# Optimization experiments

Measured on AMD Instinct MI355X. Metric: run time of the kernel, lower is better.

## Reference

```python
import jax, jax.numpy as jnp
import numpy as np

B, S, H = 32, 4096, 1024


def setup_inputs() -> dict:
    key = jax.random.key(0)
    k1, k2, k3, k4 = jax.random.split(key, 4)
    hidden = jax.random.normal(k1, (B, 1, H), dtype=jnp.float32)
    encoder_outputs = jax.random.normal(k2, (B, S, H), dtype=jnp.float32)
    # nn.Linear(H, H): weight [H, H], bias [H]; scaled like torch default-ish init
    W = jax.random.normal(k3, (H, H), dtype=jnp.float32) / np.sqrt(H)
    b = jax.random.normal(k4, (H,), dtype=jnp.float32) / np.sqrt(H)
    return {"hidden": hidden, "encoder_outputs": encoder_outputs, "W": W, "b": b}


def reference(hidden, encoder_outputs, W, b):
    # method == 'general': energy_i = Linear(enc_i); score_i = hidden[:,0] . energy_i
    energy = jnp.einsum('bsh,kh->bsk', encoder_outputs, W) + b  # [B,S,H]
    attn_energies = jnp.einsum('bh,bsh->bs', hidden[:, 0], energy)  # [B,S]
    return jax.nn.softmax(attn_energies, axis=1)
```

## Files before the change

kernel.cpp:

```cpp
#include <hip/hip_runtime.h>
#include <math.h>

#define BB 32
#define SS 4096
#define HH 1024

__global__ __launch_bounds__(256) void compute_v_kernel(
        const float* __restrict__ hidden,
        const float* __restrict__ W,
        float* __restrict__ v) {
    const int b = blockIdx.y;
    const int h = blockIdx.x * 256 + threadIdx.x;
    const float* __restrict__ hb = hidden + b * HH;
    float acc = 0.f;
#pragma unroll 8
    for (int k = 0; k < HH; ++k) {
        acc = fmaf(hb[k], W[(size_t)k * HH + h], acc);
    }
    v[b * HH + h] = acc;
}

__global__ __launch_bounds__(256) void compute_scores_kernel(
        const float* __restrict__ enc,
        const float* __restrict__ v,
        float* __restrict__ scores) {
    const int b = blockIdx.y;
    const int wave = threadIdx.x >> 6;
    const int lane = threadIdx.x & 63;
    const int s = blockIdx.x * 4 + wave;

    const float4* __restrict__ e4 =
        (const float4*)(enc + ((size_t)b * SS + s) * HH);
    const float4* __restrict__ v4 = (const float4*)(v + b * HH);

    float acc = 0.f;
#pragma unroll
    for (int i = 0; i < 4; ++i) {
        float4 e = e4[i * 64 + lane];
        float4 w = v4[i * 64 + lane];
        acc += e.x * w.x + e.y * w.y + e.z * w.z + e.w * w.w;
    }
#pragma unroll
    for (int off = 32; off > 0; off >>= 1)
        acc += __shfl_down(acc, off, 64);
    if (lane == 0) scores[(size_t)b * SS + s] = acc;
}

__global__ __launch_bounds__(256) void softmax_kernel(float* __restrict__ scores) {
    const int b = blockIdx.x;
    float* __restrict__ row = scores + (size_t)b * SS;
    const int tid = threadIdx.x;
    const int lane = tid & 63;
    const int wave = tid >> 6;

    __shared__ float red_max[4];
    __shared__ float red_sum[4];

    float vals[16];
    float m = -INFINITY;
#pragma unroll
    for (int i = 0; i < 16; ++i) {
        vals[i] = row[i * 256 + tid];
        m = fmaxf(m, vals[i]);
    }
#pragma unroll
    for (int off = 32; off > 0; off >>= 1)
        m = fmaxf(m, __shfl_down(m, off, 64));
    if (lane == 0) red_max[wave] = m;
    __syncthreads();
    m = fmaxf(fmaxf(red_max[0], red_max[1]), fmaxf(red_max[2], red_max[3]));

    float sum = 0.f;
#pragma unroll
    for (int i = 0; i < 16; ++i) {
        vals[i] = __expf(vals[i] - m);
        sum += vals[i];
    }
#pragma unroll
    for (int off = 32; off > 0; off >>= 1)
        sum += __shfl_down(sum, off, 64);
    if (lane == 0) red_sum[wave] = sum;
    __syncthreads();
    sum = red_sum[0] + red_sum[1] + red_sum[2] + red_sum[3];

    const float inv = 1.f / sum;
#pragma unroll
    for (int i = 0; i < 16; ++i)
        row[i * 256 + tid] = vals[i] * inv;
}

extern "C" void kernel_launch(void* const* d_in, const int* in_sizes, int n_in,
                              void* d_out, int out_size, void* d_ws, size_t ws_size,
                              hipStream_t stream) {
    const float* hidden = (const float*)d_in[0];
    const float* enc    = (const float*)d_in[1];
    const float* W      = (const float*)d_in[2];
    float* out = (float*)d_out;
    float* v   = (float*)d_ws;

    compute_v_kernel<<<dim3(HH / 256, BB), 256, 0, stream>>>(hidden, W, v);
    compute_scores_kernel<<<dim3(SS / 4, BB), 256, 0, stream>>>(enc, v, out);
    softmax_kernel<<<BB, 256, 0, stream>>>(out);
}
```

Baseline: 741.9 us.

## Split-K the v projection with atomics and batch rows per wave in scoring

```diff
diff --git a/kernel.cpp b/kernel.cpp
--- a/kernel.cpp
+++ b/kernel.cpp
@@ -5,19 +5,22 @@
 #define SS 4096
 #define HH 1024
 
+typedef float fvec4 __attribute__((ext_vector_type(4)));
+
 __global__ __launch_bounds__(256) void compute_v_kernel(
         const float* __restrict__ hidden,
         const float* __restrict__ W,
         float* __restrict__ v) {
     const int b = blockIdx.y;
     const int h = blockIdx.x * 256 + threadIdx.x;
-    const float* __restrict__ hb = hidden + b * HH;
+    const int k0 = blockIdx.z * 128;
+    const float* __restrict__ hb = hidden + b * HH + k0;
+    const float* __restrict__ Wp = W + (size_t)k0 * HH + h;
     float acc = 0.f;
 #pragma unroll 8
-    for (int k = 0; k < HH; ++k) {
-        acc = fmaf(hb[k], W[(size_t)k * HH + h], acc);
-    }
-    v[b * HH + h] = acc;
+    for (int k = 0; k < 128; ++k)
+        acc = fmaf(hb[k], Wp[(size_t)k * HH], acc);
+    atomicAdd(&v[b * HH + h], acc);
 }
 
 __global__ __launch_bounds__(256) void compute_scores_kernel(
@@ -27,66 +30,84 @@
     const int b = blockIdx.y;
     const int wave = threadIdx.x >> 6;
     const int lane = threadIdx.x & 63;
-    const int s = blockIdx.x * 4 + wave;
+    const int s0 = (blockIdx.x * 4 + wave) * 4;
 
-    const float4* __restrict__ e4 =
-        (const float4*)(enc + ((size_t)b * SS + s) * HH);
-    const float4* __restrict__ v4 = (const float4*)(v + b * HH);
+    const fvec4* __restrict__ v4 = (const fvec4*)(v + b * HH);
+    const fvec4 w0 = v4[lane];
+    const fvec4 w1 = v4[64 + lane];
+    const fvec4 w2 = v4[128 + lane];
+    const fvec4 w3 = v4[192 + lane];
 
-    float acc = 0.f;
+    const fvec4* __restrict__ e4 =
+        (const fvec4*)(enc + ((size_t)b * SS + s0) * HH);
+
+    float acc[4];
 #pragma unroll
-    for (int i = 0; i < 4; ++i) {
-        float4 e = e4[i * 64 + lane];
-        float4 w = v4[i * 64 + lane];
-        acc += e.x * w.x + e.y * w.y + e.z * w.z + e.w * w.w;
+    for (int j = 0; j < 4; ++j) {
+        const fvec4* __restrict__ p = e4 + (size_t)j * 256;
+        fvec4 e0 = p[lane];
+        fvec4 e1 = p[64 + lane];
+        fvec4 e2 = p[128 + lane];
+        fvec4 e3 = p[192 + lane];
+        fvec4 t = e0 * w0 + e1 * w1 + e2 * w2 + e3 * w3;
+        acc[j] = t.x + t.y + t.z + t.w;
     }
 #pragma unroll
-    for (int off = 32; off > 0; off >>= 1)
-        acc += __shfl_down(acc, off, 64);
-    if (lane == 0) scores[(size_t)b * SS + s] = acc;
+    for (int j = 0; j < 4; ++j) {
+#pragma unroll
+        for (int off = 32; off > 0; off >>= 1)
+            acc[j] += __shfl_xor(acc[j], off, 64);
+    }
+    if (lane == 0) {
+        fvec4 r = {acc[0], acc[1], acc[2], acc[3]};
+        *(fvec4*)(scores + (size_t)b * SS + s0) = r;
+    }
 }
 
-__global__ __launch_bounds__(256) void softmax_kernel(float* __restrict__ scores) {
+__global__ __launch_bounds__(1024) void softmax_kernel(float* __restrict__ scores) {
     const int b = blockIdx.x;
     float* __restrict__ row = scores + (size_t)b * SS;
     const int tid = threadIdx.x;
     const int lane = tid & 63;
     const int wave = tid >> 6;
 
-    __shared__ float red_max[4];
-    __shared__ float red_sum[4];
+    __shared__ float red_max[16];
+    __shared__ float red_sum[16];
 
-    float vals[16];
+    float vals[4];
     float m = -INFINITY;
 #pragma unroll
-    for (int i = 0; i < 16; ++i) {
-        vals[i] = row[i * 256 + tid];
+    for (int i = 0; i < 4; ++i) {
+        vals[i] = row[i * 1024 + tid];
         m = fmaxf(m, vals[i]);
     }
 #pragma unroll
     for (int off = 32; off > 0; off >>= 1)
-        m = fmaxf(m, __shfl_down(m, off, 64));
+        m = fmaxf(m, __shfl_xor(m, off, 64));
     if (lane == 0) red_max[wave] = m;
     __syncthreads();
-    m = fmaxf(fmaxf(red_max[0], red_max[1]), fmaxf(red_max[2], red_max[3]));
+#pragma unroll
+    for (int i = 0; i < 16; ++i) m = fmaxf(m, red_max[i]);
 
     float sum = 0.f;
 #pragma unroll
-    for (int i = 0; i < 16; ++i) {
+    for (int i = 0; i < 4; ++i) {
         vals[i] = __expf(vals[i] - m);
         sum += vals[i];
     }
 #pragma unroll
     for (int off = 32; off > 0; off >>= 1)
-        sum += __shfl_down(sum, off, 64);
+        sum += __shfl_xor(sum, off, 64);
     if (lane == 0) red_sum[wave] = sum;
     __syncthreads();
-    sum = red_sum[0] + red_sum[1] + red_sum[2] + red_sum[3];
+    sum = 0.f;
+#pragma unroll
+    for (int i = 0; i < 16; ++i) sum += red_sum[i];
 
     const float inv = 1.f / sum;
 #pragma unroll
-    for (int i = 0; i < 16; ++i)
-        row[i * 256 + tid] = vals[i] * inv;
+    for (int i = 0; i < 4; ++i)
+        row[i * 1024 + tid] = vals[i] * inv;
 }
 
 extern "C" void kernel_launch(void* const* d_in, const int* in_sizes, int n_in,
@@ -98,7 +119,8 @@
     float* out = (float*)d_out;
     float* v   = (float*)d_ws;
 
-    compute_v_kernel<<<dim3(HH / 256, BB), 256, 0, stream>>>(hidden, W, v);
-    compute_scores_kernel<<<dim3(SS / 4, BB), 256, 0, stream>>>(enc, v, out);
-    softmax_kernel<<<BB, 256, 0, stream>>>(out);
+    hipMemsetAsync(v, 0, (size_t)BB * HH * sizeof(float), stream);
+    compute_v_kernel<<<dim3(HH / 256, BB, 8), 256, 0, stream>>>(hidden, W, v);
+    compute_scores_kernel<<<dim3(SS / 16, BB), 256, 0, stream>>>(enc, v, out);
+    softmax_kernel<<<BB, 1024, 0, stream>>>(out);
 }
```

New measurement: 689.5 us. 7.1% less time.
